# Kernel tuning notes

Hardware: AMD Instinct MI355X
Metric: run time of the kernel (lower is better)

The kernel has to match this reference:

```python
import jax, jax.numpy as jnp
import numpy as np

R = 2048          # num residues
APR = 8           # atoms per residue -> num_atoms = 16384
H = 512           # hidden_dim (out_channels)
HEADS = 4
HD = H // HEADS
SD = HEADS * 7    # spatial feature dim
# atom_name2id: N=0, CA=1, C=2, O=3, CB=4, ...


def _layer_norm(x, g, b, eps=1e-5):
    mu = jnp.mean(x, axis=-1, keepdims=True)
    var = jnp.mean((x - mu) ** 2, axis=-1, keepdims=True)
    return (x - mu) / jnp.sqrt(var + eps) * g + b


def setup_inputs() -> dict:
    key = jax.random.key(0)
    ks = jax.random.split(key, 8)
    A = R * APR
    node_features = jax.random.normal(ks[0], (A, H), dtype=jnp.float32)
    node_positions = jax.random.normal(ks[1], (A, 3), dtype=jnp.float32) * 10.0
    # each residue owns APR consecutive atoms with types N,CA,C,O,CB,CG,CD,CE
    atom_type_ids = jnp.tile(jnp.arange(APR, dtype=jnp.int32), R)
    atom2residue = jnp.repeat(jnp.arange(R, dtype=jnp.int32), APR)
    s = 1.0 / np.sqrt(H)
    so = 1.0 / np.sqrt(H + SD)
    return {
        'node_features': node_features,
        'node_positions': node_positions,
        'Wq': jax.random.normal(ks[2], (H, H), jnp.float32) * s,
        'bq': jnp.zeros((H,), jnp.float32),
        'Wk': jax.random.normal(ks[3], (H, H), jnp.float32) * s,
        'bk': jnp.zeros((H,), jnp.float32),
        'Wv': jax.random.normal(ks[4], (H, H), jnp.float32) * s,
        'bv': jnp.zeros((H,), jnp.float32),
        'Wo': jax.random.normal(ks[5], (H + SD, H), jnp.float32) * so,
        'bo': jnp.zeros((H,), jnp.float32),
        'ln1_g': jnp.ones((H,), jnp.float32),
        'ln1_b': jnp.zeros((H,), jnp.float32),
        'ln2_g': jnp.ones((H,), jnp.float32),
        'ln2_b': jnp.zeros((H,), jnp.float32),
        'atom_type_ids': atom_type_ids,
        'atom2residue': atom2residue,
    }


def reference(node_features, node_positions, Wq, bq, Wk, bk, Wv, bv, Wo, bo,
              ln1_g, ln1_b, ln2_g, ln2_b, atom_type_ids, atom2residue):
    dt = node_features.dtype
    # ---------------- AtomPositionGather (vectorized scatter/gather) ----------------
    w_ca = (atom_type_ids == 1).astype(dt)   # CA
    w_cb = (atom_type_ids == 4).astype(dt)   # CB
    # scatter-mean of CA features per residue
    feat_sum = jax.ops.segment_sum(node_features * w_ca[:, None], atom2residue, num_segments=R)
    ca_cnt = jax.ops.segment_sum(w_ca, atom2residue, num_segments=R)
    residue_features = feat_sum / jnp.maximum(ca_cnt, 1.0)[:, None]
    # gather CA / CB positions (one CA/CB per residue in the data)
    pos_CA = jax.ops.segment_sum(node_positions * w_ca[:, None], atom2residue, num_segments=R)
    pos_CB = jax.ops.segment_sum(node_positions * w_cb[:, None], atom2residue, num_segments=R)
    no_cb = jnp.sum(jnp.abs(pos_CB), axis=1) < 1e-6
    pos_CB = jnp.where(no_cb[:, None], pos_CA, pos_CB)
    # residue completeness: >=3 atoms and contains N, CA, C
    cnt = jax.ops.segment_sum(jnp.ones_like(w_ca), atom2residue, num_segments=R)
    has = lambda t: jax.ops.segment_sum((atom_type_ids == t).astype(jnp.int32), atom2residue, num_segments=R) > 0
    residue_mask = (cnt >= 3) & has(0) & has(1) & has(2)
    # ---------------- per-residue local frames ----------------
    e1 = pos_CB - pos_CA
    n1 = jnp.linalg.norm(e1, axis=-1, keepdims=True)
    e1u = jnp.where(n1 > 1e-6, e1 / jnp.maximum(n1, 1e-6), e1)
    z_ax = jnp.array([0.0, 0.0, 1.0], dtype=dt)
    y_ax = jnp.array([0.0, 1.0, 0.0], dtype=dt)
    e2a = jnp.cross(e1u, jnp.broadcast_to(z_ax, e1u.shape))
    n2a = jnp.linalg.norm(e2a, axis=-1, keepdims=True)
    e2b = jnp.cross(e1u, jnp.broadcast_to(y_ax, e1u.shape))
    n2b = jnp.linalg.norm(e2b, axis=-1, keepdims=True)
    use_b = n2a < 1e-6
    e2 = jnp.where(use_b, e2b, e2a)
    n2 = jnp.where(use_b, n2b, n2a)
    e2u = e2 / jnp.maximum(n2, 1e-6)
    e3 = jnp.cross(e1u, e2u)
    frame = jnp.stack([e1u, e2u, e3], axis=-1)  # [R,3,3], basis as columns
    # original torch loop skips the last residue (i < len-1) and degenerate e1/e2
    ok = (jnp.arange(R) < R - 1) & (n1[:, 0] > 1e-6) & (n2[:, 0] > 1e-6)
    frames = jnp.where(ok[:, None, None], frame, jnp.eye(3, dtype=dt))
    # ---------------- PositionAwareLayer (batch=1, eval mode) ----------------
    x = residue_features[None]           # [1,R,H]
    ca = pos_CA[None]; cb = pos_CB[None]
    fr = frames[None]; m = residue_mask[None]
    q = (x @ Wq + bq).reshape(1, R, HEADS, HD)
    k = (x @ Wk + bk).reshape(1, R, HEADS, HD)
    v = (x @ Wv + bv).reshape(1, R, HEADS, HD)
    logits = jnp.einsum('blhd,bkhd->blkh', q, k)
    m2 = (m[:, :, None] & m[:, None, :])[..., None]          # [1,R,R,1]
    logits = jnp.where(m2, logits, -jnp.inf)
    alpha = jax.nn.softmax(logits, axis=2)                    # softmax over k
    feat_node = jnp.einsum('blkh,bkhd->blhd', alpha, v).reshape(1, R, H)
    rel_pos = cb[:, :, None, :] - ca[:, None, :, :]           # CB[l]-CA[k]: [1,R,R,3]
    bias = jnp.einsum('blkh,blkd->blhd', alpha, rel_pos)      # [1,R,HEADS,3]
    dist = jnp.linalg.norm(bias, axis=-1, keepdims=True)
    pts = jnp.einsum('blij,blhj->blhi', fr, bias)
    dirn = pts / (jnp.linalg.norm(pts, axis=-1, keepdims=True) + 1e-10)
    feat_spatial = jnp.concatenate([pts.reshape(1, R, -1), dist.reshape(1, R, -1), dirn.reshape(1, R, -1)], axis=-1)
    feat_all = jnp.concatenate([feat_node, feat_spatial], axis=-1)  # [1,R,H+SD]
    h = jax.nn.relu(feat_all @ Wo + bo)                       # dropout = identity (eval)
    h = _layer_norm(h, ln1_g, ln1_b)
    h = jnp.where(m[..., None], h, jnp.zeros_like(h))
    x_updated = _layer_norm(x + h, ln2_g, ln2_b)
    return x_updated
```

## Files before the change

### kernel.cpp

```cpp
#include <hip/hip_runtime.h>
#include <hip/hip_bf16.h>
#include <stdint.h>


#define R_ 2048
#define APR_ 8
#define H_ 512
#define HEADS_ 4
#define HD_ 128
#define FA_LD 544

typedef __attribute__((ext_vector_type(4))) float f32x4;
typedef __attribute__((ext_vector_type(4))) unsigned int u32x4;
typedef __attribute__((ext_vector_type(4))) unsigned short us4;
typedef __bf16 bf16x8 __attribute__((ext_vector_type(8)));

static __device__ __forceinline__ float bf2f(unsigned short u) {
    union { unsigned int i; float f; } c; c.i = ((unsigned int)u) << 16; return c.f;
}
static __device__ __forceinline__ unsigned short f2bf(float f) {
    union { float f; unsigned int i; } c; c.f = f;
    unsigned int r = c.i + 0x7fffu + ((c.i >> 16) & 1u);
    return (unsigned short)(r >> 16);
}
static __device__ __forceinline__ float loadf(const void* p, size_t i, bool f32) {
    float v = f32 ? ((const float*)p)[i] : bf2f(((const unsigned short*)p)[i]);
    return (v == v && fabsf(v) < 1e30f) ? v : 0.f;
}

__global__ void diag(unsigned short* out, float val) {
    if (threadIdx.x == 0 && blockIdx.x == 0) out[0] = f2bf(val);
}

__global__ void detect_dtype(const unsigned short* __restrict__ nf, int* flag) {
    __shared__ int bad;
    if (threadIdx.x == 0) bad = 0;
    __syncthreads();
    int cnt = 0;
    for (int i = threadIdx.x; i < 8192; i += 256) {
        unsigned e = (nf[i] >> 7) & 0xFFu;
        if (e >= 0xC0u) cnt++;
    }
    atomicAdd(&bad, cnt);
    __syncthreads();
    if (threadIdx.x == 0) *flag = (bad > 16) ? 1 : 0;
}

__global__ void gather_frames(const void* __restrict__ pos,
                              const int* __restrict__ atype,
                              const int* __restrict__ flag,
                              int* __restrict__ cai, float* __restrict__ ca,
                              float* __restrict__ cb, float* __restrict__ fr,
                              float* __restrict__ maskf, f32x4* __restrict__ ca4)
{
    int r = blockIdx.x * blockDim.x + threadIdx.x;
    if (r >= R_) return;
    bool f32 = *flag != 0;
    int base = r * APR_;
    float caP[3] = {0,0,0}, cbP[3] = {0,0,0};
    int idx = base; bool h0=false, h1=false, h2=false;
    for (int a = 0; a < APR_; a++) {
        int t = atype[base + a];
        if (t == 0) h0 = true;
        if (t == 2) h2 = true;
        if (t == 1) { h1 = true; idx = base + a;
            for (int j = 0; j < 3; j++) caP[j] += loadf(pos, (size_t)(base+a)*3 + j, f32); }
        if (t == 4) {
            for (int j = 0; j < 3; j++) cbP[j] += loadf(pos, (size_t)(base+a)*3 + j, f32); }
    }
    float s = fabsf(cbP[0]) + fabsf(cbP[1]) + fabsf(cbP[2]);
    if (s < 1e-6f) { cbP[0]=caP[0]; cbP[1]=caP[1]; cbP[2]=caP[2]; }
    float e1[3] = { cbP[0]-caP[0], cbP[1]-caP[1], cbP[2]-caP[2] };
    float n1 = sqrtf(e1[0]*e1[0] + e1[1]*e1[1] + e1[2]*e1[2]);
    float e1u[3] = { e1[0], e1[1], e1[2] };
    if (n1 > 1e-6f) { float iv = 1.f / fmaxf(n1, 1e-6f); e1u[0]*=iv; e1u[1]*=iv; e1u[2]*=iv; }
    float e2a[3] = { e1u[1], -e1u[0], 0.f };
    float n2a = sqrtf(e2a[0]*e2a[0] + e2a[1]*e2a[1]);
    float e2b[3] = { -e1u[2], 0.f, e1u[0] };
    float n2b = sqrtf(e2b[0]*e2b[0] + e2b[2]*e2b[2]);
    bool useb = n2a < 1e-6f;
    float e2[3] = { useb?e2b[0]:e2a[0], useb?e2b[1]:e2a[1], useb?e2b[2]:e2a[2] };
    float n2 = useb ? n2b : n2a;
    float iv2 = 1.f / fmaxf(n2, 1e-6f);
    float e2u[3] = { e2[0]*iv2, e2[1]*iv2, e2[2]*iv2 };
    float e3[3] = { e1u[1]*e2u[2]-e1u[2]*e2u[1],
                    e1u[2]*e2u[0]-e1u[0]*e2u[2],
                    e1u[0]*e2u[1]-e1u[1]*e2u[0] };
    bool ok = (r < R_-1) && (n1 > 1e-6f) && (n2 > 1e-6f);
    float F[9];
    if (ok) { F[0]=e1u[0]; F[1]=e2u[0]; F[2]=e3[0];
              F[3]=e1u[1]; F[4]=e2u[1]; F[5]=e3[1];
              F[6]=e1u[2]; F[7]=e2u[2]; F[8]=e3[2]; }
    else    { F[0]=1;F[1]=0;F[2]=0; F[3]=0;F[4]=1;F[5]=0; F[6]=0;F[7]=0;F[8]=1; }
    cai[r] = idx;
    for (int j = 0; j < 3; j++) { ca[r*3+j] = caP[j]; cb[r*3+j] = cbP[j]; }
    for (int j = 0; j < 9; j++) fr[r*9+j] = F[j];
    float mk = (h0 && h1 && h2) ? 1.f : 0.f;
    maskf[r] = mk;
    f32x4 c4; c4[0]=caP[0]; c4[1]=caP[1]; c4[2]=caP[2]; c4[3]=mk;
    ca4[r] = c4;
}

__global__ __launch_bounds__(256) void pack_prep(
    const void* __restrict__ nf, const int* __restrict__ cai,
    const void* __restrict__ Wq, const void* __restrict__ Wk, const void* __restrict__ Wv,
    const void* __restrict__ Wo,
    unsigned short* __restrict__ xg_hi, unsigned short* __restrict__ xg_lo,
    unsigned short* __restrict__ wqt_hi, unsigned short* __restrict__ wqt_lo,
    unsigned short* __restrict__ wot_hi, unsigned short* __restrict__ wot_lo,
    const int* __restrict__ flag)
{
    const bool f32 = *flag != 0;
    const int bid = blockIdx.x, tid = threadIdx.x;
    us4 h4, l4;
    if (bid < 1024) {
        int flat = bid*256 + tid;
        int row = flat >> 7, kc = flat & 127;
        size_t src = (size_t)cai[row]*H_ + kc*4;
        #pragma unroll
        for (int i = 0; i < 4; i++) {
            float v = loadf(nf, src + i, f32);
            unsigned short hb = f2bf(v);
            h4[i] = hb; l4[i] = f2bf(v - bf2f(hb));
        }
        *(us4*)(xg_hi + (size_t)row*H_ + kc*4) = h4;
        *(us4*)(xg_lo + (size_t)row*H_ + kc*4) = l4;
    } else if (bid < 1792) {
        int flat = (bid-1024)*256 + tid;
        int kc = flat / 1536, nn = flat - kc*1536;
        int mat = nn >> 9, ncol = nn & 511;
        const void* W = (mat==0) ? Wq : (mat==1) ? Wk : Wv;
        #pragma unroll
        for (int i = 0; i < 4; i++) {
            float v = loadf(W, (size_t)(kc*4+i)*H_ + ncol, f32);
            unsigned short hb = f2bf(v);
            h4[i] = hb; l4[i] = f2bf(v - bf2f(hb));
        }
        *(us4*)(wqt_hi + (size_t)nn*H_ + kc*4) = h4;
        *(us4*)(wqt_lo + (size_t)nn*H_ + kc*4) = l4;
    } else {
        int flat = (bid-1792)*256 + tid;
        int kc = flat >> 9, n = flat & 511;
        #pragma unroll
        for (int i = 0; i < 4; i++) {
            int k = kc*4 + i;
            float v = (k < 540) ? loadf(Wo, (size_t)k*H_ + n, f32) : 0.f;
            unsigned short hb = f2bf(v);
            h4[i] = hb; l4[i] = f2bf(v - bf2f(hb));
        }
        *(us4*)(wot_hi + (size_t)n*FA_LD + kc*4) = h4;
        *(us4*)(wot_lo + (size_t)n*FA_LD + kc*4) = l4;
    }
}

__global__ __launch_bounds__(256) void qkv_mfma(
    const unsigned short* __restrict__ xg_hi, const unsigned short* __restrict__ xg_lo,
    const unsigned short* __restrict__ wqt_hi, const unsigned short* __restrict__ wqt_lo,
    const void* __restrict__ bq, const void* __restrict__ bk, const void* __restrict__ bv,
    unsigned short* __restrict__ qf, unsigned short* __restrict__ kf,
    unsigned short* __restrict__ vt, const int* __restrict__ flag)
{
    __shared__ __align__(16) char smem[17408];
    char* Xhi = smem;
    char* Xlo = smem + 4096;
    char* Bhi = smem + 8192;
    char* Blo = smem + 12288;
    const int tid = threadIdx.x;
    const int w = tid >> 6, lane = tid & 63, cL = lane & 15, gL = lane >> 4;
    const int wm = w >> 1, wn = w & 1;
    const int mbase = blockIdx.x * 64;
    const int nblk  = blockIdx.y * 64;
    const int mat = nblk >> 9, ncol0 = nblk & 511;
    const bool f32 = *flag != 0;
    const unsigned short* ahg = xg_hi + (size_t)mbase * H_;
    const unsigned short* alg = xg_lo + (size_t)mbase * H_;
    const unsigned short* bhg = wqt_hi + (size_t)nblk * H_;
    const unsigned short* blg = wqt_lo + (size_t)nblk * H_;

    u32x4 va[2], vb[2];
#define QKV_LOAD(K0)                                                          \
    {                                                                         \
        _Pragma("unroll")                                                     \
        for (int i = 0; i < 2; i++) {                                         \
            int flat = i*256 + tid, pl = flat >> 8, rem = flat & 255;         \
            int row = rem >> 2, c16 = rem & 3;                                \
            const unsigned short* pa = pl ? alg : ahg;                        \
            va[i] = *(const u32x4*)(pa + (size_t)row*H_ + (K0) + c16*8);      \
        }                                                                     \
        _Pragma("unroll")                                                     \
        for (int i = 0; i < 2; i++) {                                         \
            int flat = i*256 + tid, pl = flat >> 8, rem = flat & 255;         \
            int row = rem >> 2, c16 = rem & 3;                                \
            const unsigned short* pb = pl ? blg : bhg;                        \
            vb[i] = *(const u32x4*)(pb + (size_t)row*H_ + (K0) + c16*8);      \
        }                                                                     \
    }
    QKV_LOAD(0)
    f32x4 acc[2][2] = {};
    for (int kt = 0; kt < 16; kt++) {
        __syncthreads();
        #pragma unroll
        for (int i = 0; i < 2; i++) {
            int flat = i*256 + tid, pl = flat >> 8, rem = flat & 255;
            int row = rem >> 2, c16 = rem & 3;
            char* p = pl ? Xlo : Xhi;
            *(u32x4*)(p + row*64 + ((c16*16) ^ (((row>>1)&3)<<4))) = va[i];
        }
        #pragma unroll
        for (int i = 0; i < 2; i++) {
            int flat = i*256 + tid, pl = flat >> 8, rem = flat & 255;
            int row = rem >> 2, c16 = rem & 3;
            char* p = pl ? Blo : Bhi;
            *(u32x4*)(p + row*64 + ((c16*16) ^ (((row>>1)&3)<<4))) = vb[i];
        }
        __syncthreads();
        if (kt < 15) QKV_LOAD((kt+1)*32)
        bf16x8 ah[2], al[2], bh[2], bl[2];
        #pragma unroll
        for (int ms = 0; ms < 2; ms++) {
            int row = wm*32 + ms*16 + cL;
            int off = row*64 + ((gL*16) ^ (((row>>1)&3)<<4));
            ah[ms] = *(const bf16x8*)(Xhi + off);
            al[ms] = *(const bf16x8*)(Xlo + off);
        }
        #pragma unroll
        for (int ns = 0; ns < 2; ns++) {
            int row = wn*32 + ns*16 + cL;
            int off = row*64 + ((gL*16) ^ (((row>>1)&3)<<4));
            bh[ns] = *(const bf16x8*)(Bhi + off);
            bl[ns] = *(const bf16x8*)(Blo + off);
        }
        #pragma unroll
        for (int ms = 0; ms < 2; ms++)
            #pragma unroll
            for (int ns = 0; ns < 2; ns++) {
                acc[ms][ns] = __builtin_amdgcn_mfma_f32_16x16x32_bf16(ah[ms], bh[ns], acc[ms][ns], 0,0,0);
                acc[ms][ns] = __builtin_amdgcn_mfma_f32_16x16x32_bf16(ah[ms], bl[ns], acc[ms][ns], 0,0,0);
                acc[ms][ns] = __builtin_amdgcn_mfma_f32_16x16x32_bf16(al[ms], bh[ns], acc[ms][ns], 0,0,0);
            }
    }
#undef QKV_LOAD
    const void* bias = (mat==0) ? bq : (mat==1) ? bk : bv;
    if (mat == 2) {
        #pragma unroll
        for (int ns = 0; ns < 2; ns++) {
            int ncol = ncol0 + wn*32 + ns*16 + cL;
            float bc = loadf(bias, ncol, f32);
            #pragma unroll
            for (int ms = 0; ms < 2; ms++) {
                int m0 = mbase + wm*32 + ms*16 + gL*4;
                us4 pk;
                #pragma unroll
                for (int j = 0; j < 4; j++) pk[j] = f2bf(acc[ms][ns][j] + bc);
                *(us4*)(vt + (size_t)ncol*R_ + m0) = pk;
            }
        }
    } else {
        unsigned short* dst = (mat==0) ? qf : kf;
        float* ep = (float*)smem + w*1088;
        __syncthreads();
        #pragma unroll
        for (int ms = 0; ms < 2; ms++)
            #pragma unroll
            for (int ns = 0; ns < 2; ns++)
                #pragma unroll
                for (int j = 0; j < 4; j++)
                    ep[(ms*16 + gL*4 + j)*34 + ns*16 + cL] = acc[ms][ns][j];
        __syncthreads();
        int r = lane >> 1, cp = (lane & 1) * 16;
        int mrow = mbase + wm*32 + r;
        #pragma unroll
        for (int c4 = 0; c4 < 4; c4++) {
            int nloc = cp + c4*4;
            int ncol = ncol0 + wn*32 + nloc;
            us4 pk;
            #pragma unroll
            for (int e = 0; e < 4; e++)
                pk[e] = f2bf(ep[r*34 + nloc + e] + loadf(bias, ncol + e, f32));
            *(us4*)(dst + (size_t)mrow*H_ + ncol) = pk;
        }
    }
}

__global__ __launch_bounds__(256) void wo_mfma(
    const float* __restrict__ fa,
    const unsigned short* __restrict__ wot_hi, const unsigned short* __restrict__ wot_lo,
    const void* __restrict__ bo, float* __restrict__ Y,
    const int* __restrict__ flag)
{
    __shared__ __align__(16) char smem[17408];
    char* Ahi = smem;
    char* Alo = smem + 4096;
    char* Bhi = smem + 8192;
    char* Blo = smem + 12288;
    const int tid = threadIdx.x;
    const int w = tid >> 6, lane = tid & 63, cL = lane & 15, gL = lane >> 4;
    const int wm = w >> 1, wn = w & 1;
    const int mbase = blockIdx.x * 64;
    const int nbase = blockIdx.y * 64;
    const bool f32 = *flag != 0;
    const unsigned short* bhg = wot_hi + (size_t)nbase * FA_LD;
    const unsigned short* blg = wot_lo + (size_t)nbase * FA_LD;

    float xv[8];
    u32x4 vb[2];
#define WO_LOAD(K0)                                                           \
    {                                                                         \
        _Pragma("unroll")                                                     \
        for (int i = 0; i < 2; i++) {                                         \
            int flat = i*256 + tid, row = flat >> 3, c4 = flat & 7;           \
            f32x4 t = *(const f32x4*)(fa + (size_t)(mbase+row)*FA_LD + (K0) + c4*4); \
            _Pragma("unroll")                                                 \
            for (int e = 0; e < 4; e++) xv[i*4+e] = t[e];                     \
        }                                                                     \
        _Pragma("unroll")                                                     \
        for (int i = 0; i < 2; i++) {                                         \
            int flat = i*256 + tid, pl = flat >> 8, rem = flat & 255;         \
            int row = rem >> 2, c16 = rem & 3;                                \
            const unsigned short* pb = pl ? blg : bhg;                        \
            vb[i] = *(const u32x4*)(pb + (size_t)row*FA_LD + (K0) + c16*8);   \
        }                                                                     \
    }
    WO_LOAD(0)
    f32x4 acc[2][2] = {};
    for (int kt = 0; kt < 17; kt++) {
        __syncthreads();
        #pragma unroll
        for (int i = 0; i < 2; i++) {
            int flat = i*256 + tid, row = flat >> 3, c4 = flat & 7;
            int sw = ((row>>1)&3) << 4;
            us4 h4, l4;
            #pragma unroll
            for (int e = 0; e < 4; e++) {
                float v = xv[i*4+e];
                unsigned short hb = f2bf(v);
                h4[e] = hb; l4[e] = f2bf(v - bf2f(hb));
            }
            *(us4*)(Ahi + row*64 + ((c4*8) ^ sw)) = h4;
            *(us4*)(Alo + row*64 + ((c4*8) ^ sw)) = l4;
        }
        #pragma unroll
        for (int i = 0; i < 2; i++) {
            int flat = i*256 + tid, pl = flat >> 8, rem = flat & 255;
            int row = rem >> 2, c16 = rem & 3;
            char* p = pl ? Blo : Bhi;
            *(u32x4*)(p + row*64 + ((c16*16) ^ (((row>>1)&3)<<4))) = vb[i];
        }
        __syncthreads();
        if (kt < 16) WO_LOAD((kt+1)*32)
        bf16x8 ah[2], al[2], bh[2], bl[2];
        #pragma unroll
        for (int ms = 0; ms < 2; ms++) {
            int row = wm*32 + ms*16 + cL;
            int off = row*64 + ((gL*16) ^ (((row>>1)&3)<<4));
            ah[ms] = *(const bf16x8*)(Ahi + off);
            al[ms] = *(const bf16x8*)(Alo + off);
        }
        #pragma unroll
        for (int ns = 0; ns < 2; ns++) {
            int row = wn*32 + ns*16 + cL;
            int off = row*64 + ((gL*16) ^ (((row>>1)&3)<<4));
            bh[ns] = *(const bf16x8*)(Bhi + off);
            bl[ns] = *(const bf16x8*)(Blo + off);
        }
        #pragma unroll
        for (int ms = 0; ms < 2; ms++)
            #pragma unroll
            for (int ns = 0; ns < 2; ns++) {
                acc[ms][ns] = __builtin_amdgcn_mfma_f32_16x16x32_bf16(ah[ms], bh[ns], acc[ms][ns], 0,0,0);
                acc[ms][ns] = __builtin_amdgcn_mfma_f32_16x16x32_bf16(ah[ms], bl[ns], acc[ms][ns], 0,0,0);
                acc[ms][ns] = __builtin_amdgcn_mfma_f32_16x16x32_bf16(al[ms], bh[ns], acc[ms][ns], 0,0,0);
            }
    }
#undef WO_LOAD
    float* ep = (float*)smem + w*1088;
    __syncthreads();
    #pragma unroll
    for (int ms = 0; ms < 2; ms++)
        #pragma unroll
        for (int ns = 0; ns < 2; ns++)
            #pragma unroll
            for (int j = 0; j < 4; j++)
                ep[(ms*16 + gL*4 + j)*34 + ns*16 + cL] = acc[ms][ns][j];
    __syncthreads();
    int r = lane >> 1, cp = (lane & 1) * 16;
    int mrow = mbase + wm*32 + r;
    #pragma unroll
    for (int c4 = 0; c4 < 4; c4++) {
        int nloc = cp + c4*4;
        int ncol = nbase + wn*32 + nloc;
        f32x4 o;
        #pragma unroll
        for (int e = 0; e < 4; e++)
            o[e] = ep[r*34 + nloc + e] + loadf(bo, ncol + e, f32);
        *(f32x4*)(Y + (size_t)mrow*H_ + ncol) = o;
    }
}

__global__ __launch_bounds__(512, 1) void attn_mfma3(
    const unsigned short* __restrict__ qf, const unsigned short* __restrict__ kf,
    const unsigned short* __restrict__ vt,
    const f32x4* __restrict__ ca4, const float* __restrict__ maskf,
    const float* __restrict__ cb, const float* __restrict__ fr,
    float* __restrict__ fa)
{
    __shared__ __align__(16) char smem[86016];
    const int tid = threadIdx.x;
    const int w = tid >> 6, lane = tid & 63;
    const int cL = lane & 15, gL = lane >> 4;
    const int qbase = blockIdx.x * 32;
    const int h = blockIdx.y;

    char* KsW  = smem + w*8192;
    char* AshW = smem + 65536 + w*2560;

    bf16x8 qfrag[2][4];
    #pragma unroll
    for (int mt = 0; mt < 2; mt++)
        #pragma unroll
        for (int ks = 0; ks < 4; ks++)
            qfrag[mt][ks] = *(const bf16x8*)(qf + (size_t)(qbase + mt*16 + cL)*H_
                                             + h*HD_ + ks*32 + gL*8);
    float mq[2][4];
    #pragma unroll
    for (int mt = 0; mt < 2; mt++)
        #pragma unroll
        for (int j = 0; j < 4; j++)
            mq[mt][j] = (maskf[qbase + mt*16 + gL*4 + j] > 0.f) ? 1.f : 0.f;

    f32x4 O[2][8] = {};
    float den[2][4] = {}, axv[2][4] = {}, ayv[2][4] = {}, azv[2][4] = {};

    const unsigned short* kbase = kf + h*HD_;
    const unsigned short* vbase = vt + (size_t)h*HD_*R_;

    for (int kt = w; kt < 64; kt += 8) {
        const int kb = kt * 32;
        u32x4 tK[8];
        #pragma unroll
        for (int j = 0; j < 8; j++) {
            int flat = j*64 + lane;
            tK[j] = *(const u32x4*)(kbase + (size_t)(kb + (flat>>4))*H_ + (flat&15)*8);
        }
        bf16x8 vreg[8];
        #pragma unroll
        for (int dt = 0; dt < 8; dt++)
            vreg[dt] = *(const bf16x8*)(vbase + (size_t)(dt*16 + cL)*R_ + kb + gL*8);
        f32x4 cav[2];
        #pragma unroll
        for (int nt = 0; nt < 2; nt++)
            cav[nt] = ca4[kb + nt*16 + cL];
        #pragma unroll
        for (int j = 0; j < 8; j++) {
            int flat = j*64 + lane;
            int row = flat>>4, c = flat&15;
            *(u32x4*)(KsW + row*256 + ((c*16) ^ ((row&7)<<4))) = tK[j];
        }
        f32x4 sacc[2][2] = {};
        #pragma unroll
        for (int nt = 0; nt < 2; nt++) {
            int n = nt*16 + cL;
            int rs = (n&7)<<4;
            bf16x8 k0 = *(const bf16x8*)(KsW + n*256 + (((0*4+gL)*16) ^ rs));
            bf16x8 k1 = *(const bf16x8*)(KsW + n*256 + (((1*4+gL)*16) ^ rs));
            bf16x8 k2 = *(const bf16x8*)(KsW + n*256 + (((2*4+gL)*16) ^ rs));
            bf16x8 k3 = *(const bf16x8*)(KsW + n*256 + (((3*4+gL)*16) ^ rs));
            #pragma unroll
            for (int mt = 0; mt < 2; mt++) {
                sacc[mt][nt] = __builtin_amdgcn_mfma_f32_16x16x32_bf16(qfrag[mt][0], k0, sacc[mt][nt], 0,0,0);
                sacc[mt][nt] = __builtin_amdgcn_mfma_f32_16x16x32_bf16(qfrag[mt][1], k1, sacc[mt][nt], 0,0,0);
                sacc[mt][nt] = __builtin_amdgcn_mfma_f32_16x16x32_bf16(qfrag[mt][2], k2, sacc[mt][nt], 0,0,0);
                sacc[mt][nt] = __builtin_amdgcn_mfma_f32_16x16x32_bf16(qfrag[mt][3], k3, sacc[mt][nt], 0,0,0);
            }
        }
        unsigned short* arow = (unsigned short*)AshW;
        #pragma unroll
        for (int nt = 0; nt < 2; nt++) {
            #pragma unroll
            for (int mt = 0; mt < 2; mt++) {
                f32x4 s4 = sacc[mt][nt];
                float av[4];
                #pragma unroll
                for (int j = 0; j < 4; j++) {
                    float a = __expf(fminf(s4[j], 75.f)) * cav[nt][3] * mq[mt][j];
                    if (!(a < 3.0e38f)) a = 0.f;
                    av[j] = a;
                    den[mt][j] += a;
                    axv[mt][j] += a * cav[nt][0];
                    ayv[mt][j] += a * cav[nt][1];
                    azv[mt][j] += a * cav[nt][2];
                }
                unsigned int p01, p23;
                asm("v_cvt_pk_bf16_f32 %0, %1, %2" : "=v"(p01) : "v"(av[0]), "v"(av[1]));
                asm("v_cvt_pk_bf16_f32 %0, %1, %2" : "=v"(p23) : "v"(av[2]), "v"(av[3]));
                int qr = mt*16 + gL*4;
                int col = nt*16 + cL;
                arow[(qr+0)*40 + col] = (unsigned short)p01;
                arow[(qr+1)*40 + col] = (unsigned short)(p01 >> 16);
                arow[(qr+2)*40 + col] = (unsigned short)p23;
                arow[(qr+3)*40 + col] = (unsigned short)(p23 >> 16);
            }
        }
        bf16x8 pa0 = *(const bf16x8*)(AshW + ((size_t)(cL)*40      + gL*8)*2);
        bf16x8 pa1 = *(const bf16x8*)(AshW + ((size_t)(16 + cL)*40 + gL*8)*2);
        #pragma unroll
        for (int dt = 0; dt < 8; dt++) {
            O[0][dt] = __builtin_amdgcn_mfma_f32_16x16x32_bf16(pa0, vreg[dt], O[0][dt], 0,0,0);
            O[1][dt] = __builtin_amdgcn_mfma_f32_16x16x32_bf16(pa1, vreg[dt], O[1][dt], 0,0,0);
        }
    }

    __syncthreads();
    float* Ored = (float*)smem;
    float* dred = (float*)(smem + 69632);
    #pragma unroll
    for (int mt = 0; mt < 2; mt++)
        #pragma unroll
        for (int j = 0; j < 4; j++) {
            float d0 = den[mt][j], x0 = axv[mt][j], y0 = ayv[mt][j], z0 = azv[mt][j];
            #pragma unroll
            for (int off = 8; off >= 1; off >>= 1) {
                d0 += __shfl_xor(d0, off); x0 += __shfl_xor(x0, off);
                y0 += __shfl_xor(y0, off); z0 += __shfl_xor(z0, off);
            }
            if (cL == 0) {
                f32x4 v; v[0]=d0; v[1]=x0; v[2]=y0; v[3]=z0;
                *(f32x4*)&dred[w*128 + (mt*16 + gL*4 + j)*4] = v;
            }
        }
    #pragma unroll
    for (int mt = 0; mt < 2; mt++)
        #pragma unroll
        for (int dtl = 0; dtl < 4; dtl++) {
            f32x4 o4 = O[mt][dtl];
            #pragma unroll
            for (int j = 0; j < 4; j++)
                Ored[w*2176 + (mt*16 + gL*4 + j)*68 + dtl*16 + cL] = o4[j];
        }
    __syncthreads();
    {
        int q = tid >> 4, c4 = (tid & 15) * 4;
        float dn = 0.f;
        #pragma unroll
        for (int ww = 0; ww < 8; ww++) dn += dred[ww*128 + q*4];
        float inv = (dn > 0.f) ? 1.f/dn : 0.f;
        f32x4 s = *(const f32x4*)&Ored[q*68 + c4];
        #pragma unroll
        for (int ww = 1; ww < 8; ww++)
            s += *(const f32x4*)&Ored[ww*2176 + q*68 + c4];
        *(f32x4*)&fa[(size_t)(qbase+q)*FA_LD + h*HD_ + c4] = s * inv;
    }
    if (tid < 32) {
        float dn=0.f, ax=0.f, ay=0.f, az=0.f;
        #pragma unroll
        for (int ww = 0; ww < 8; ww++) {
            const float* dp = &dred[ww*128 + tid*4];
            dn += dp[0]; ax += dp[1]; ay += dp[2]; az += dp[3];
        }
        float inv = (dn > 0.f) ? 1.f/dn : 0.f;
        float live = (dn > 0.f) ? 1.f : 0.f;
        int qg = qbase + tid;
        float b0 = cb[qg*3+0]*live - ax*inv;
        float b1 = cb[qg*3+1]*live - ay*inv;
        float b2 = cb[qg*3+2]*live - az*inv;
        float dist = sqrtf(b0*b0 + b1*b1 + b2*b2);
        const float* F = fr + (size_t)qg*9;
        float p0 = F[0]*b0 + F[1]*b1 + F[2]*b2;
        float p1 = F[3]*b0 + F[4]*b1 + F[5]*b2;
        float p2 = F[6]*b0 + F[7]*b1 + F[8]*b2;
        float pn = sqrtf(p0*p0 + p1*p1 + p2*p2) + 1e-10f;
        size_t rb = (size_t)qg * FA_LD;
        fa[rb + 512 + h*3 + 0] = p0;
        fa[rb + 512 + h*3 + 1] = p1;
        fa[rb + 512 + h*3 + 2] = p2;
        fa[rb + 524 + h]       = dist;
        fa[rb + 528 + h*3 + 0] = p0/pn;
        fa[rb + 528 + h*3 + 1] = p1/pn;
        fa[rb + 528 + h*3 + 2] = p2/pn;
        if (h == 0) { fa[rb+540]=0.f; fa[rb+541]=0.f; fa[rb+542]=0.f; fa[rb+543]=0.f; }
    }
    __syncthreads();
    #pragma unroll
    for (int mt = 0; mt < 2; mt++)
        #pragma unroll
        for (int dtl = 0; dtl < 4; dtl++) {
            f32x4 o4 = O[mt][4 + dtl];
            #pragma unroll
            for (int j = 0; j < 4; j++)
                Ored[w*2176 + (mt*16 + gL*4 + j)*68 + dtl*16 + cL] = o4[j];
        }
    __syncthreads();
    {
        int q = tid >> 4, c4 = (tid & 15) * 4;
        float dn = 0.f;
        #pragma unroll
        for (int ww = 0; ww < 8; ww++) dn += dred[ww*128 + q*4];
        float inv = (dn > 0.f) ? 1.f/dn : 0.f;
        f32x4 s = *(const f32x4*)&Ored[q*68 + c4];
        #pragma unroll
        for (int ww = 1; ww < 8; ww++)
            s += *(const f32x4*)&Ored[ww*2176 + q*68 + c4];
        *(f32x4*)&fa[(size_t)(qbase+q)*FA_LD + h*HD_ + 64 + c4] = s * inv;
    }
}

__global__ __launch_bounds__(256) void final_ln(
    const float* __restrict__ Y, const void* __restrict__ nf,
    const int* __restrict__ cai, const float* __restrict__ maskf,
    const void* __restrict__ g1, const void* __restrict__ b1,
    const void* __restrict__ g2, const void* __restrict__ b2,
    void* __restrict__ out, const int* __restrict__ flag)
{
    const int tid = threadIdx.x, lane = tid & 63, wave = tid >> 6;
    const int r = blockIdx.x * 4 + wave;
    bool f32 = *flag != 0;
    const float mk = maskf[r];
    const size_t xrow = (size_t)cai[r] * H_;
    float y[8], s1 = 0.f, s2 = 0.f;
    #pragma unroll
    for (int i = 0; i < 8; i++) {
        int c = lane + i*64;
        float v = fmaxf(Y[(size_t)r*H_ + c], 0.f);
        y[i] = v; s1 += v; s2 += v*v;
    }
    #pragma unroll
    for (int off = 32; off; off >>= 1) { s1 += __shfl_xor(s1, off); s2 += __shfl_xor(s2, off); }
    float mu = s1 * (1.f/H_);
    float var = s2 * (1.f/H_) - mu*mu;
    float rstd = rsqrtf(fmaxf(var, 0.f) + 1e-5f);
    float t[8], u1 = 0.f, u2 = 0.f;
    #pragma unroll
    for (int i = 0; i < 8; i++) {
        int c = lane + i*64;
        float hh = (y[i]-mu)*rstd*loadf(g1, c, f32) + loadf(b1, c, f32);
        hh *= mk;
        float tv = loadf(nf, xrow + c, f32) + hh;
        t[i] = tv; u1 += tv; u2 += tv*tv;
    }
    #pragma unroll
    for (int off = 32; off; off >>= 1) { u1 += __shfl_xor(u1, off); u2 += __shfl_xor(u2, off); }
    float mu2 = u1 * (1.f/H_);
    float var2 = u2 * (1.f/H_) - mu2*mu2;
    float rstd2 = rsqrtf(fmaxf(var2, 0.f) + 1e-5f);
    #pragma unroll
    for (int i = 0; i < 8; i++) {
        int c = lane + i*64;
        float ov = (t[i]-mu2)*rstd2*loadf(g2, c, f32) + loadf(b2, c, f32);
        if (f32) ((float*)out)[(size_t)r*H_ + c] = ov;
        else ((unsigned short*)out)[(size_t)r*H_ + c] = f2bf(ov);
    }
}

extern "C" void kernel_launch(void* const* d_in, const int* in_sizes, int n_in,
                              void* d_out, int out_size, void* d_ws, size_t ws_size,
                              hipStream_t stream)
{
    static const int expected[16] = {
        8388608, 49152, 262144, 512, 262144, 512, 262144, 512,
        276480, 512, 512, 512, 512, 512, 16384, 16384
    };
    if (n_in != 16) {
        diag<<<dim3(1), dim3(64), 0, stream>>>((unsigned short*)d_out, 1000.f + n_in);
        return;
    }
    for (int i = 0; i < 16; i++) {
        if (in_sizes[i] != expected[i]) {
            diag<<<dim3(1), dim3(64), 0, stream>>>((unsigned short*)d_out, 2000.f + 10.f*i);
            return;
        }
    }
    const size_t need = 16056320;
    if (ws_size < need) {
        diag<<<dim3(1), dim3(64), 0, stream>>>((unsigned short*)d_out, 3000.f);
        return;
    }

    const void* nf  = d_in[0];
    const void* pos = d_in[1];
    const void* Wq  = d_in[2];  const void* bq = d_in[3];
    const void* Wk  = d_in[4];  const void* bk = d_in[5];
    const void* Wv  = d_in[6];  const void* bv = d_in[7];
    const void* Wo  = d_in[8];  const void* bo = d_in[9];
    const void* g1  = d_in[10]; const void* b1 = d_in[11];
    const void* g2  = d_in[12]; const void* b2 = d_in[13];
    const int* atype = (const int*)d_in[14];

    char* ws = (char*)d_ws;
    int*   flag  = (int*)  (ws + 0);
    int*   cai   = (int*)  (ws + 1024);
    float* ca    = (float*)(ws + 9216);
    float* cb    = (float*)(ws + 33792);
    float* fr    = (float*)(ws + 58368);
    float* maskf = (float*)(ws + 132096);
    f32x4* ca4   = (f32x4*)(ws + 140288);
    unsigned short* qf = (unsigned short*)(ws + 1048576);
    unsigned short* kf = (unsigned short*)(ws + 3145728);
    unsigned short* vt = (unsigned short*)(ws + 5242880);
    unsigned short* xg_hi = (unsigned short*)(ws + 7340032);
    unsigned short* xg_lo = (unsigned short*)(ws + 9437184);
    float* fa = (float*)(ws + 7340032);
    unsigned short* wqt_hi = (unsigned short*)(ws + 11796480);
    unsigned short* wqt_lo = (unsigned short*)(ws + 13369344);
    unsigned short* wot_hi = (unsigned short*)(ws + 14942208);
    unsigned short* wot_lo = (unsigned short*)(ws + 15499264);
    float* Y  = (float*)qf;

    detect_dtype<<<dim3(1), dim3(256), 0, stream>>>((const unsigned short*)nf, flag);
    gather_frames<<<dim3(8), dim3(256), 0, stream>>>(pos, atype, flag, cai, ca, cb, fr,
                                                     maskf, ca4);
    pack_prep<<<dim3(2064), dim3(256), 0, stream>>>(nf, cai, Wq, Wk, Wv, Wo,
                                                    xg_hi, xg_lo, wqt_hi, wqt_lo,
                                                    wot_hi, wot_lo, flag);
    qkv_mfma<<<dim3(32, 24), dim3(256), 0, stream>>>(xg_hi, xg_lo, wqt_hi, wqt_lo,
                                                     bq, bk, bv, qf, kf, vt, flag);
    attn_mfma3<<<dim3(R_/32, HEADS_), dim3(512), 0, stream>>>(qf, kf, vt, ca4, maskf,
                                                              cb, fr, fa);
    wo_mfma<<<dim3(32, 8), dim3(256), 0, stream>>>(fa, wot_hi, wot_lo, bo, Y, flag);
    final_ln<<<dim3(512), dim3(256), 0, stream>>>(Y, nf, cai, maskf, g1, b1, g2, b2,
                                                  d_out, flag);
}
```

Measured before the change: 188.8 us.

## Split attention over key halves and merge partials in a finalize kernel

The attention kernel grid gains a z dimension of 2. Each block now handles half of the keys (4 tiles per wave instead of 8) and writes unnormalized partial outputs and denominators to workspace. A new finalize kernel sums the two halves, normalizes, and computes the spatial features. K fragments are also loaded straight from global memory into registers instead of being staged through swizzled LDS. The goal is to double the block count from 256 to 512 so the GPU is better filled, at the cost of an extra launch and a partial-buffer round trip.

```diff
diff --git a/kernel.cpp b/kernel.cpp
--- a/kernel.cpp
+++ b/kernel.cpp
@@ -397,22 +397,20 @@
     }
 }
 
-__global__ __launch_bounds__(512, 1) void attn_mfma3(
+__global__ __launch_bounds__(512, 1) void attn_mfma4(
     const unsigned short* __restrict__ qf, const unsigned short* __restrict__ kf,
     const unsigned short* __restrict__ vt,
     const f32x4* __restrict__ ca4, const float* __restrict__ maskf,
-    const float* __restrict__ cb, const float* __restrict__ fr,
-    float* __restrict__ fa)
+    float* __restrict__ po, float* __restrict__ pd)
 {
-    __shared__ __align__(16) char smem[86016];
+    __shared__ __align__(16) char smem[73728];
     const int tid = threadIdx.x;
     const int w = tid >> 6, lane = tid & 63;
     const int cL = lane & 15, gL = lane >> 4;
     const int qbase = blockIdx.x * 32;
     const int h = blockIdx.y;
-
-    char* KsW  = smem + w*8192;
-    char* AshW = smem + 65536 + w*2560;
+    const int s = blockIdx.z;
+    char* AshW = smem + w*2560;
 
     bf16x8 qfrag[2][4];
     #pragma unroll
@@ -434,45 +432,36 @@
     const unsigned short* kbase = kf + h*HD_;
     const unsigned short* vbase = vt + (size_t)h*HD_*R_;
 
-    for (int kt = w; kt < 64; kt += 8) {
+    #pragma unroll
+    for (int i = 0; i < 4; i++) {
+        const int kt = s*32 + w + i*8;
         const int kb = kt * 32;
-        u32x4 tK[8];
-        #pragma unroll
-        for (int j = 0; j < 8; j++) {
-            int flat = j*64 + lane;
-            tK[j] = *(const u32x4*)(kbase + (size_t)(kb + (flat>>4))*H_ + (flat&15)*8);
+        bf16x8 kfr[2][4];
+        #pragma unroll
+        for (int nt = 0; nt < 2; nt++) {
+            const unsigned short* kr = kbase + (size_t)(kb + nt*16 + cL)*H_ + gL*8;
+            kfr[nt][0] = *(const bf16x8*)(kr);
+            kfr[nt][1] = *(const bf16x8*)(kr + 32);
+            kfr[nt][2] = *(const bf16x8*)(kr + 64);
+            kfr[nt][3] = *(const bf16x8*)(kr + 96);
         }
         bf16x8 vreg[8];
         #pragma unroll
         for (int dt = 0; dt < 8; dt++)
             vreg[dt] = *(const bf16x8*)(vbase + (size_t)(dt*16 + cL)*R_ + kb + gL*8);
         f32x4 cav[2];
+        cav[0] = ca4[kb + cL];
+        cav[1] = ca4[kb + 16 + cL];
+        f32x4 sacc[2][2] = {};
         #pragma unroll
         for (int nt = 0; nt < 2; nt++)
-            cav[nt] = ca4[kb + nt*16 + cL];
-        #pragma unroll
-        for (int j = 0; j < 8; j++) {
-            int flat = j*64 + lane;
-            int row = flat>>4, c = flat&15;
-            *(u32x4*)(KsW + row*256 + ((c*16) ^ ((row&7)<<4))) = tK[j];
-        }
-        f32x4 sacc[2][2] = {};
-        #pragma unroll
-        for (int nt = 0; nt < 2; nt++) {
-            int n = nt*16 + cL;
-            int rs = (n&7)<<4;
-            bf16x8 k0 = *(const bf16x8*)(KsW + n*256 + (((0*4+gL)*16) ^ rs));
-            bf16x8 k1 = *(const bf16x8*)(KsW + n*256 + (((1*4+gL)*16) ^ rs));
-            bf16x8 k2 = *(const bf16x8*)(KsW + n*256 + (((2*4+gL)*16) ^ rs));
-            bf16x8 k3 = *(const bf16x8*)(KsW + n*256 + (((3*4+gL)*16) ^ rs));
             #pragma unroll
             for (int mt = 0; mt < 2; mt++) {
-                sacc[mt][nt] = __builtin_amdgcn_mfma_f32_16x16x32_bf16(qfrag[mt][0], k0, sacc[mt][nt], 0,0,0);
-                sacc[mt][nt] = __builtin_amdgcn_mfma_f32_16x16x32_bf16(qfrag[mt][1], k1, sacc[mt][nt], 0,0,0);
-                sacc[mt][nt] = __builtin_amdgcn_mfma_f32_16x16x32_bf16(qfrag[mt][2], k2, sacc[mt][nt], 0,0,0);
-                sacc[mt][nt] = __builtin_amdgcn_mfma_f32_16x16x32_bf16(qfrag[mt][3], k3, sacc[mt][nt], 0,0,0);
+                sacc[mt][nt] = __builtin_amdgcn_mfma_f32_16x16x32_bf16(qfrag[mt][0], kfr[nt][0], sacc[mt][nt], 0,0,0);
+                sacc[mt][nt] = __builtin_amdgcn_mfma_f32_16x16x32_bf16(qfrag[mt][1], kfr[nt][1], sacc[mt][nt], 0,0,0);
+                sacc[mt][nt] = __builtin_amdgcn_mfma_f32_16x16x32_bf16(qfrag[mt][2], kfr[nt][2], sacc[mt][nt], 0,0,0);
+                sacc[mt][nt] = __builtin_amdgcn_mfma_f32_16x16x32_bf16(qfrag[mt][3], kfr[nt][3], sacc[mt][nt], 0,0,0);
             }
-        }
         unsigned short* arow = (unsigned short*)AshW;
         #pragma unroll
         for (int nt = 0; nt < 2; nt++) {
@@ -538,69 +527,95 @@
                 Ored[w*2176 + (mt*16 + gL*4 + j)*68 + dtl*16 + cL] = o4[j];
         }
     __syncthreads();
+    const size_t pbase = ((size_t)(s*64 + blockIdx.x)*4 + h)*32;
     {
         int q = tid >> 4, c4 = (tid & 15) * 4;
-        float dn = 0.f;
-        #pragma unroll
-        for (int ww = 0; ww < 8; ww++) dn += dred[ww*128 + q*4];
-        float inv = (dn > 0.f) ? 1.f/dn : 0.f;
-        f32x4 s = *(const f32x4*)&Ored[q*68 + c4];
+        f32x4 sum = *(const f32x4*)&Ored[q*68 + c4];
         #pragma unroll
         for (int ww = 1; ww < 8; ww++)
-            s += *(const f32x4*)&Ored[ww*2176 + q*68 + c4];
-        *(f32x4*)&fa[(size_t)(qbase+q)*FA_LD + h*HD_ + c4] = s * inv;
+            sum += *(const f32x4*)&Ored[ww*2176 + q*68 + c4];
+        *(f32x4*)&po[(pbase + q)*128 + c4] = sum;
+    }
+    if (tid < 128) {
+        int q = tid >> 2, c = tid & 3;
+        float v = 0.f;
+        #pragma unroll
+        for (int ww = 0; ww < 8; ww++) v += dred[ww*128 + q*4 + c];
+        pd[(pbase + q)*4 + c] = v;
+    }
+    __syncthreads();
+    #pragma unroll
+    for (int mt = 0; mt < 2; mt++)
+        #pragma unroll
+        for (int dtl = 0; dtl < 4; dtl++) {
+            f32x4 o4 = O[mt][4 + dtl];
+            #pragma unroll
+            for (int j = 0; j < 4; j++)
+                Ored[w*2176 + (mt*16 + gL*4 + j)*68 + dtl*16 + cL] = o4[j];
+        }
+    __syncthreads();
+    {
+        int q = tid >> 4, c4 = (tid & 15) * 4;
+        f32x4 sum = *(const f32x4*)&Ored[q*68 + c4];
+        #pragma unroll
+        for (int ww = 1; ww < 8; ww++)
+            sum += *(const f32x4*)&Ored[ww*2176 + q*68 + c4];
+        *(f32x4*)&po[(pbase + q)*128 + 64 + c4] = sum;
+    }
+}
+
+__global__ __launch_bounds__(256) void finalize_attn(
+    const float* __restrict__ po, const float* __restrict__ pd,
+    const float* __restrict__ cb, const float* __restrict__ fr,
+    float* __restrict__ fa)
+{
+    __shared__ float invs[32];
+    __shared__ float dsum[32][4];
+    const int tid = threadIdx.x;
+    const int qb = blockIdx.x, h = blockIdx.y;
+    const size_t p0 = ((size_t)(qb)*4 + h)*32;
+    const size_t p1 = ((size_t)(64 + qb)*4 + h)*32;
+    if (tid < 128) {
+        int q = tid >> 2, c = tid & 3;
+        float v = pd[(p0 + q)*4 + c] + pd[(p1 + q)*4 + c];
+        dsum[q][c] = v;
+        if (c == 0) invs[q] = (v > 0.f) ? 1.f/v : 0.f;
+    }
+    __syncthreads();
+    {
+        int q = tid >> 3, d0 = (tid & 7) * 16;
+        float inv = invs[q];
+        size_t rowb = (size_t)(qb*32 + q)*FA_LD + h*HD_ + d0;
+        #pragma unroll
+        for (int e = 0; e < 4; e++) {
+            f32x4 a = *(const f32x4*)&po[(p0 + q)*128 + d0 + e*4];
+            f32x4 b = *(const f32x4*)&po[(p1 + q)*128 + d0 + e*4];
+            *(f32x4*)&fa[rowb + e*4] = (a + b) * inv;
+        }
     }
     if (tid < 32) {
-        float dn=0.f, ax=0.f, ay=0.f, az=0.f;
-        #pragma unroll
-        for (int ww = 0; ww < 8; ww++) {
-            const float* dp = &dred[ww*128 + tid*4];
-            dn += dp[0]; ax += dp[1]; ay += dp[2]; az += dp[3];
-        }
+        float dn = dsum[tid][0], ax = dsum[tid][1], ay = dsum[tid][2], az = dsum[tid][3];
         float inv = (dn > 0.f) ? 1.f/dn : 0.f;
         float live = (dn > 0.f) ? 1.f : 0.f;
-        int qg = qbase + tid;
+        int qg = qb*32 + tid;
         float b0 = cb[qg*3+0]*live - ax*inv;
         float b1 = cb[qg*3+1]*live - ay*inv;
         float b2 = cb[qg*3+2]*live - az*inv;
         float dist = sqrtf(b0*b0 + b1*b1 + b2*b2);
         const float* F = fr + (size_t)qg*9;
-        float p0 = F[0]*b0 + F[1]*b1 + F[2]*b2;
-        float p1 = F[3]*b0 + F[4]*b1 + F[5]*b2;
-        float p2 = F[6]*b0 + F[7]*b1 + F[8]*b2;
-        float pn = sqrtf(p0*p0 + p1*p1 + p2*p2) + 1e-10f;
+        float p0f = F[0]*b0 + F[1]*b1 + F[2]*b2;
+        float p1f = F[3]*b0 + F[4]*b1 + F[5]*b2;
+        float p2f = F[6]*b0 + F[7]*b1 + F[8]*b2;
+        float pn = sqrtf(p0f*p0f + p1f*p1f + p2f*p2f) + 1e-10f;
         size_t rb = (size_t)qg * FA_LD;
-        fa[rb + 512 + h*3 + 0] = p0;
-        fa[rb + 512 + h*3 + 1] = p1;
-        fa[rb + 512 + h*3 + 2] = p2;
+        fa[rb + 512 + h*3 + 0] = p0f;
+        fa[rb + 512 + h*3 + 1] = p1f;
+        fa[rb + 512 + h*3 + 2] = p2f;
         fa[rb + 524 + h]       = dist;
-        fa[rb + 528 + h*3 + 0] = p0/pn;
-        fa[rb + 528 + h*3 + 1] = p1/pn;
-        fa[rb + 528 + h*3 + 2] = p2/pn;
+        fa[rb + 528 + h*3 + 0] = p0f/pn;
+        fa[rb + 528 + h*3 + 1] = p1f/pn;
+        fa[rb + 528 + h*3 + 2] = p2f/pn;
         if (h == 0) { fa[rb+540]=0.f; fa[rb+541]=0.f; fa[rb+542]=0.f; fa[rb+543]=0.f; }
-    }
-    __syncthreads();
-    #pragma unroll
-    for (int mt = 0; mt < 2; mt++)
-        #pragma unroll
-        for (int dtl = 0; dtl < 4; dtl++) {
-            f32x4 o4 = O[mt][4 + dtl];
-            #pragma unroll
-            for (int j = 0; j < 4; j++)
-                Ored[w*2176 + (mt*16 + gL*4 + j)*68 + dtl*16 + cL] = o4[j];
-        }
-    __syncthreads();
-    {
-        int q = tid >> 4, c4 = (tid & 15) * 4;
-        float dn = 0.f;
-        #pragma unroll
-        for (int ww = 0; ww < 8; ww++) dn += dred[ww*128 + q*4];
-        float inv = (dn > 0.f) ? 1.f/dn : 0.f;
-        f32x4 s = *(const f32x4*)&Ored[q*68 + c4];
-        #pragma unroll
-        for (int ww = 1; ww < 8; ww++)
-            s += *(const f32x4*)&Ored[ww*2176 + q*68 + c4];
-        *(f32x4*)&fa[(size_t)(qbase+q)*FA_LD + h*HD_ + 64 + c4] = s * inv;
     }
 }
 
@@ -669,7 +684,7 @@
             return;
         }
     }
-    const size_t need = 16056320;
+    const size_t need = 25427968;
     if (ws_size < need) {
         diag<<<dim3(1), dim3(64), 0, stream>>>((unsigned short*)d_out, 3000.f);
         return;
@@ -703,6 +718,8 @@
     unsigned short* wqt_lo = (unsigned short*)(ws + 13369344);
     unsigned short* wot_hi = (unsigned short*)(ws + 14942208);
     unsigned short* wot_lo = (unsigned short*)(ws + 15499264);
+    float* po = (float*)(ws + 16777216);
+    float* pd = (float*)(ws + 25165824);
     float* Y  = (float*)qf;
 
     detect_dtype<<<dim3(1), dim3(256), 0, stream>>>((const unsigned short*)nf, flag);
@@ -713,8 +730,9 @@
                                                     wot_hi, wot_lo, flag);
     qkv_mfma<<<dim3(32, 24), dim3(256), 0, stream>>>(xg_hi, xg_lo, wqt_hi, wqt_lo,
                                                      bq, bk, bv, qf, kf, vt, flag);
-    attn_mfma3<<<dim3(R_/32, HEADS_), dim3(512), 0, stream>>>(qf, kf, vt, ca4, maskf,
-                                                              cb, fr, fa);
+    attn_mfma4<<<dim3(R_/32, HEADS_, 2), dim3(512), 0, stream>>>(qf, kf, vt, ca4, maskf,
+                                                                 po, pd);
+    finalize_attn<<<dim3(R_/32, HEADS_), dim3(256), 0, stream>>>(po, pd, cb, fr, fa);
     wo_mfma<<<dim3(32, 8), dim3(256), 0, stream>>>(fa, wot_hi, wot_lo, bo, Y, flag);
     final_ln<<<dim3(512), dim3(256), 0, stream>>>(Y, nf, cai, maskf, g1, b1, g2, b2,
                                                   d_out, flag);
```

Result: slower. 216.2 us (+14.5%).
